# Kernel optimization log

Hardware: AMD Instinct MI355X
Metric: run time of the kernel (lower is better)

Reference implementation:

```python
import jax, jax.numpy as jnp
import numpy as np

N = 4096        # atoms
F = 128         # node feature channels (MACE hidden irreps scalar channels)
K = 8           # radial basis size
NELEM = 10      # chemical elements
RMAX = 5.0      # cutoff (Angstrom), model.r_max
BOX = 34.5      # box side -> ~0.1 atoms/A^3, ~50 neighbors within RMAX


def setup_inputs() -> dict:
    key = jax.random.key(0)
    ks = jax.random.split(key, 7)
    positions = jax.random.uniform(ks[0], (N, 3), jnp.float32) * BOX
    z = jax.random.randint(ks[1], (N,), 0, NELEM)
    embed = jax.random.normal(ks[2], (NELEM, F), jnp.float32) * 0.1
    W1 = jax.random.normal(ks[3], (K, F, F), jnp.float32) / np.sqrt(K * F)
    W2 = jax.random.normal(ks[4], (K, F, F), jnp.float32) / np.sqrt(K * F)
    Wr1 = jax.random.normal(ks[5], (F, F), jnp.float32) / np.sqrt(F)
    Wr2 = jax.random.normal(ks[6], (F, 1), jnp.float32) / np.sqrt(F)
    return dict(positions=positions, z=z, embed=embed, W1=W1, W2=W2, Wr1=Wr1, Wr2=Wr2)


def _energy(positions, embed, W1, W2, Wr1, Wr2, z):
    # node embedding from atomic species (node_attrs one-hot @ embedding)
    h = embed[z]                                            # [N,F]
    # --- neighborlist: radius graph with self-edge masking (pbc = False) ---
    sq = jnp.sum(positions * positions, axis=-1)            # [N]
    d2 = sq[:, None] + sq[None, :] - 2.0 * (positions @ positions.T)  # [N,N]
    eye = jnp.eye(positions.shape[0], dtype=bool)
    d2_safe = jnp.where(eye | (d2 <= 0), 1.0, d2)           # avoid sqrt(0) grad
    d = jnp.sqrt(d2_safe)                                   # [N,N]
    mask = (d < RMAX) & (~eye) & (d2 > 0)                   # keep_edge = ~true_self_edge
    # smooth cutoff envelope
    env = jnp.where(mask, 0.5 * (jnp.cos(jnp.pi * d / RMAX) + 1.0), 0.0)  # [N,N]
    # Gaussian radial basis
    mus = jnp.linspace(0.0, RMAX, K, dtype=jnp.float32)     # [K]
    gamma = jnp.float32((K / RMAX) ** 2)
    rbf = jnp.exp(-gamma * (d[..., None] - mus) ** 2) * env[..., None]    # [N,N,K]
    # --- two message-passing layers (radial-weighted neighbor aggregation) ---
    for W in (W1, W2):
        A = jnp.einsum('ijk,jf->ikf', rbf, h)               # [N,K,F] gather-scatter agg
        h = jax.nn.silu(jnp.einsum('ikf,kfg->ig', A, W) + h)  # [N,F]
    # --- per-atom energy readout, summed over graph ---
    e_atom = (jax.nn.silu(h @ Wr1) @ Wr2)[:, 0]             # [N]
    return jnp.sum(e_atom)


def reference(positions, z, embed, W1, W2, Wr1, Wr2):
    energy, dE_dpos = jax.value_and_grad(_energy)(positions, embed, W1, W2, Wr1, Wr2, z)
    forces = -dE_dpos                                       # [N,3]
    return energy, forces
```

## Files before the change

kernel.cpp:

```cpp
#include <hip/hip_runtime.h>
#include <math.h>

#define N_ATOMS 4096
#define F 128
#define K 8
#define KF 1024
#define KFF 131072
#define FF 16384
#define NF 524288
#define NKF 4194304
#define MAXNB 128
#define RMAX 5.0f
#define GAMMA 2.56f
#define MU_STEP 0.714285714285714f
#define PI_F 3.14159265358979323846f
#define POR (PI_F / RMAX)

typedef __bf16 bf16x8_t __attribute__((ext_vector_type(8)));
typedef float f32x4_t __attribute__((ext_vector_type(4)));
typedef unsigned short u16x8_t __attribute__((ext_vector_type(8)));
typedef unsigned short u16x4_t __attribute__((ext_vector_type(4)));

__device__ __forceinline__ float sigm(float x){ return 1.0f/(1.0f + expf(-x)); }
__device__ __forceinline__ unsigned short f2bf(float x){
  unsigned int u = __float_as_uint(x);
  u += 0x7fff + ((u >> 16) & 1);
  return (unsigned short)(u >> 16);
}


__device__ __forceinline__ void agg_body(int a, int t,
        const float* __restrict__ h_in, const int* __restrict__ nb_idx,
        const float* __restrict__ rbf, const int* __restrict__ nb_cnt,
        unsigned short* __restrict__ Af){
  int grp = t >> 6, lane = t & 63;
  __shared__ int s_j[MAXNB];
  __shared__ float s_acc[4][8][128];
  int cnt = nb_cnt[a];
  for (int idx = t; idx < cnt; idx += 256) s_j[idx] = nb_idx[a*MAXNB + idx];
  __syncthreads();
  float2 acc[8];
  #pragma unroll
  for (int k = 0; k < 8; k++) acc[k] = {0.f, 0.f};
  const float4* rb = (const float4*)(rbf + (size_t)a*MAXNB*8);
  for (int n = grp; n < cnt; n += 4){
    float2 hv = *(const float2*)&h_in[(size_t)s_j[n]*F + lane*2];
    float4 r0 = rb[n*2], r1 = rb[n*2+1];
    acc[0].x += r0.x*hv.x; acc[0].y += r0.x*hv.y;
    acc[1].x += r0.y*hv.x; acc[1].y += r0.y*hv.y;
    acc[2].x += r0.z*hv.x; acc[2].y += r0.z*hv.y;
    acc[3].x += r0.w*hv.x; acc[3].y += r0.w*hv.y;
    acc[4].x += r1.x*hv.x; acc[4].y += r1.x*hv.y;
    acc[5].x += r1.y*hv.x; acc[5].y += r1.y*hv.y;
    acc[6].x += r1.z*hv.x; acc[6].y += r1.z*hv.y;
    acc[7].x += r1.w*hv.x; acc[7].y += r1.w*hv.y;
  }
  #pragma unroll
  for (int k = 0; k < 8; k++)
    *(float2*)&s_acc[grp][k][lane*2] = acc[k];
  __syncthreads();
  int k = t >> 5, q = t & 31;
  int f0 = q*4;
  float v[4];
  #pragma unroll
  for (int i = 0; i < 4; i++){
    int f = f0 + i;
    v[i] = s_acc[0][k][f] + s_acc[1][k][f] + s_acc[2][k][f] + s_acc[3][k][f];
  }
  int lf = (a & 15) | (((f0 >> 3) & 3) << 4);
  int kc = k*4 + (f0 >> 5);
  size_t flat = (size_t)(a >> 4)*16384 + ((size_t)kc*64 + lf)*8 + (f0 & 7);
  u16x4_t o;
  o[0] = f2bf(v[0]); o[1] = f2bf(v[1]); o[2] = f2bf(v[2]); o[3] = f2bf(v[3]);
  *(u16x4_t*)(Af + flat) = o;
}

__device__ __forceinline__ void mgemm_bwd_body(int bx, int t,
        const unsigned short* __restrict__ Gf, const unsigned short* __restrict__ Bf,
        unsigned short* __restrict__ dAbf){
  int l = t & 63, w = t >> 6;
  int rtile = (bx & 63)*4 + w;
  int nt0 = (bx >> 6)*8;
  f32x4_t acc[8];
  #pragma unroll
  for (int i = 0; i < 8; i++) acc[i] = (f32x4_t){0.f,0.f,0.f,0.f};
  const unsigned short* Ab = Gf + (size_t)rtile*2048 + l*8;
  const unsigned short* Bb = Bf + l*8;
  #pragma unroll
  for (int kc = 0; kc < 4; kc++){
    bf16x8_t a = *(const bf16x8_t*)(Ab + kc*512);
    #pragma unroll
    for (int nt = 0; nt < 8; nt++){
      bf16x8_t b = *(const bf16x8_t*)(Bb + (kc*64 + nt0 + nt)*512);
      acc[nt] = __builtin_amdgcn_mfma_f32_16x16x32_bf16(a, b, acc[nt], 0, 0, 0);
    }
  }
  int row0 = rtile*16 + (l >> 4)*4;
  int col = l & 15;
  #pragma unroll
  for (int nt = 0; nt < 8; nt++){
    #pragma unroll
    for (int r = 0; r < 4; r++)
      dAbf[(size_t)(row0+r)*1024 + (nt0+nt)*16 + col] = f2bf(acc[nt][r]);
  }
}


__global__ __launch_bounds__(256) void k_prep(const float* __restrict__ pos,
        const int* __restrict__ z, const float* __restrict__ embed,
        const float* __restrict__ W1, const float* __restrict__ W2,
        const float* __restrict__ Wr1,
        int* __restrict__ nb_idx, float* __restrict__ nb_d, int* __restrict__ nb_cnt,
        float* __restrict__ rbf, float* __restrict__ drbf,
        unsigned short* __restrict__ WF1, unsigned short* __restrict__ WF2,
        unsigned short* __restrict__ WDF2, unsigned short* __restrict__ WTF1,
        unsigned short* __restrict__ WTF2, unsigned short* __restrict__ Wr1F,
        unsigned short* __restrict__ Wr1TF,
        float* __restrict__ h0, unsigned short* __restrict__ h0bf){
  int t = threadIdx.x;
  if (blockIdx.x < 1024){
    int w = t >> 6, lane = t & 63;
    int i = blockIdx.x*4 + w;
    __shared__ float spx[256], spy[256], spz[256], ssq[256];
    float pix = pos[3*i], piy = pos[3*i+1], piz = pos[3*i+2];
    float sqi = pix*pix + piy*piy + piz*piz;
    int count = 0;
    for (int jb = 0; jb < N_ATOMS; jb += 256){
      __syncthreads();
      float px = pos[3*(jb+t)], py = pos[3*(jb+t)+1], pz = pos[3*(jb+t)+2];
      spx[t] = px; spy[t] = py; spz[t] = pz;
      ssq[t] = px*px + py*py + pz*pz;
      __syncthreads();
      #pragma unroll
      for (int c = 0; c < 4; c++){
        int jj = c*64 + lane;
        int j = jb + jj;
        float dot = pix*spx[jj] + piy*spy[jj] + piz*spz[jj];
        float d2 = sqi + ssq[jj] - 2.0f*dot;
        float d = sqrtf(d2);
        bool pred = (j != i) && (d2 > 0.0f) && (d < RMAX);
        unsigned long long m = __ballot(pred);
        int off = __popcll(m & ((1ull << lane) - 1ull));
        if (pred){
          int p = count + off;
          if (p < MAXNB){ nb_idx[i*MAXNB + p] = j; nb_d[i*MAXNB + p] = d; }
        }
        count += __popcll(m);
      }
    }
    int cc = count > MAXNB ? MAXNB : count;
    if (lane == 0) nb_cnt[i] = cc;
    __syncthreads();
    for (int n = lane; n < cc; n += 64){
      float d = nb_d[i*MAXNB + n];
      float ph = POR*d;
      float cph, sph;
      __sincosf(ph, &sph, &cph);
      float env = 0.5f*(cph + 1.0f);
      float denv = -0.5f*POR*sph;
      float rr[8], dd[8];
      #pragma unroll
      for (int k = 0; k < 8; k++){
        float dm = d - MU_STEP*(float)k;
        float G = expf(-GAMMA*dm*dm);
        rr[k] = G*env;
        dd[k] = G*(-2.0f*GAMMA*dm*env + denv);
      }
      float4* rb = (float4*)(rbf + ((size_t)i*MAXNB + n)*8);
      rb[0] = {rr[0],rr[1],rr[2],rr[3]};
      rb[1] = {rr[4],rr[5],rr[6],rr[7]};
      float4* db = (float4*)(drbf + ((size_t)i*MAXNB + n)*8);
      db[0] = {dd[0],dd[1],dd[2],dd[3]};
      db[1] = {dd[4],dd[5],dd[6],dd[7]};
    }
    return;
  }
  if (blockIdx.x >= 1088){
    int idx = (blockIdx.x - 1088)*256 + t;
    int i = idx >> 7, f = idx & 127;
    float v = embed[z[i]*F + f];
    h0[idx] = v;
    h0bf[idx] = f2bf(v);
    return;
  }
  int idx = (blockIdx.x - 1024)*256 + t;
  int l = idx & 63;
  int hi = idx >> 6;
  {
    int kc = hi >> 3, nt = hi & 7;
    int kfb = kc*32 + ((l>>4)&3)*8;
    int g = nt*16 + (l&15);
    u16x8_t v1, v2, vd;
    #pragma unroll
    for (int j = 0; j < 8; j++){
      int kf = kfb + j;
      v1[j] = f2bf(W1[kf*128 + g]);
      v2[j] = f2bf(W2[kf*128 + g]);
      vd[j] = f2bf(W2[(kf>>7)*FF + g*F + (kf&127)]);
    }
    *(u16x8_t*)(WF1 + idx*8) = v1;
    *(u16x8_t*)(WF2 + idx*8) = v2;
    *(u16x8_t*)(WDF2 + idx*8) = vd;
  }
  {
    int kc = hi >> 6, nt = hi & 63;
    int gb = kc*32 + ((l>>4)&3)*8;
    int kf = nt*16 + (l&15);
    u16x8_t t1, t2;
    #pragma unroll
    for (int j = 0; j < 8; j++){
      int g = gb + j;
      t1[j] = f2bf(W1[kf*128 + g]);
      t2[j] = f2bf(W2[kf*128 + g]);
    }
    *(u16x8_t*)(WTF1 + idx*8) = t1;
    *(u16x8_t*)(WTF2 + idx*8) = t2;
  }
  {
    int m = idx >> 9;
    int ll = (idx >> 3) & 63;
    int j = idx & 7;
    int kc = m >> 3, nt = m & 7;
    int kf = kc*32 + ((ll>>4)&3)*8 + j;
    int g = nt*16 + (ll&15);
    Wr1F[idx]  = f2bf(Wr1[kf*128 + g]);
    Wr1TF[idx] = f2bf(Wr1[g*128 + kf]);
  }
}

__global__ __launch_bounds__(256) void k_agg(const float* __restrict__ h_in,
        const int* __restrict__ nb_idx, const float* __restrict__ rbf,
        const int* __restrict__ nb_cnt, unsigned short* __restrict__ Af){
  agg_body(blockIdx.x, threadIdx.x, h_in, nb_idx, rbf, nb_cnt, Af);
}

__global__ __launch_bounds__(256) void k_bwdmix(const unsigned short* __restrict__ Gf,
        const unsigned short* __restrict__ Bf, unsigned short* __restrict__ dAbf,
        const float* __restrict__ g2b, const int* __restrict__ nb_idx,
        const float* __restrict__ rbf, const int* __restrict__ nb_cnt,
        unsigned short* __restrict__ Af){
  if (blockIdx.x < 512){
    mgemm_bwd_body(blockIdx.x, threadIdx.x, Gf, Bf, dAbf);
    return;
  }
  agg_body(blockIdx.x - 512, threadIdx.x, g2b, nb_idx, rbf, nb_cnt, Af);
}

__global__ __launch_bounds__(256) void k_mgemm_bwd(const unsigned short* __restrict__ Gf,
        const unsigned short* __restrict__ Bf, unsigned short* __restrict__ dAbf){
  mgemm_bwd_body(blockIdx.x, threadIdx.x, Gf, Bf, dAbf);
}

__global__ __launch_bounds__(256) void k_mgemm_fwd(const unsigned short* __restrict__ Af,
        const unsigned short* __restrict__ Bf, const float* __restrict__ addv,
        const float* __restrict__ msrc, float* __restrict__ out_m,
        float* __restrict__ out_h, unsigned short* __restrict__ out_hbf,
        unsigned short* __restrict__ out_frag, int mode){
  int t = threadIdx.x;
  int l = t & 63, w = t >> 6;
  int rtile = blockIdx.x;
  int nt = blockIdx.y*4 + w;
  f32x4_t accA = (f32x4_t){0.f,0.f,0.f,0.f};
  f32x4_t accB = (f32x4_t){0.f,0.f,0.f,0.f};
  const unsigned short* Ab = Af + (size_t)rtile*16384 + l*8;
  const unsigned short* Bb = Bf + l*8;
  #pragma unroll
  for (int kc = 0; kc < 32; kc += 2){
    bf16x8_t a0 = *(const bf16x8_t*)(Ab + kc*512);
    bf16x8_t b0 = *(const bf16x8_t*)(Bb + (kc*8 + nt)*512);
    bf16x8_t a1 = *(const bf16x8_t*)(Ab + (kc+1)*512);
    bf16x8_t b1 = *(const bf16x8_t*)(Bb + ((kc+1)*8 + nt)*512);
    accA = __builtin_amdgcn_mfma_f32_16x16x32_bf16(a0, b0, accA, 0, 0, 0);
    accB = __builtin_amdgcn_mfma_f32_16x16x32_bf16(a1, b1, accB, 0, 0, 0);
  }
  f32x4_t acc = accA + accB;
  int row0 = rtile*16 + (l >> 4)*4;
  int col = nt*16 + (l & 15);
  if (mode == 0){
    #pragma unroll
    for (int r = 0; r < 4; r++){
      int i = row0 + r;
      float m = acc[r] + addv[(size_t)i*F + col];
      out_m[(size_t)i*F + col] = m;
      float h = m*sigm(m);
      out_h[(size_t)i*F + col] = h;
      out_hbf[(size_t)i*F + col] = f2bf(h);
    }
  } else {
    int kc2 = col >> 5;
    int lfr0 = (((col >> 3) & 3) << 4);
    int jj = col & 7;
    #pragma unroll
    for (int r = 0; r < 4; r++){
      int i = row0 + r;
      float mm = msrc[(size_t)i*F + col];
      float sg = sigm(mm);
      float gv = (acc[r] + addv[(size_t)i*F + col])*(sg*(1.f + mm*(1.f - sg)));
      int lfr = (i & 15) | lfr0;
      size_t flat = (((size_t)(i>>4)*4 + kc2)*64 + lfr)*8 + jj;
      out_frag[flat] = f2bf(gv);
    }
  }
}

__global__ __launch_bounds__(64) void k_readout(const unsigned short* __restrict__ h2bf,
        const float* __restrict__ m2, const unsigned short* __restrict__ Wr1F,
        const unsigned short* __restrict__ Wr1TF, const float* __restrict__ Wr2,
        float* __restrict__ e_at, float* __restrict__ g2,
        unsigned short* __restrict__ g2frag){
  int a0 = blockIdx.x*16;
  int l = threadIdx.x;
  int rl = l & 15;
  __shared__ unsigned short sdu[16][136];
  f32x4_t acc[8];
  #pragma unroll
  for (int nt = 0; nt < 8; nt++) acc[nt] = (f32x4_t){0.f,0.f,0.f,0.f};
  #pragma unroll
  for (int kc = 0; kc < 4; kc++){
    bf16x8_t af = *(const bf16x8_t*)(h2bf + (size_t)(a0+rl)*F + kc*32 + ((l>>4)&3)*8);
    #pragma unroll
    for (int nt = 0; nt < 8; nt++){
      bf16x8_t bf = *(const bf16x8_t*)(Wr1F + ((kc*8+nt)*64 + l)*8);
      acc[nt] = __builtin_amdgcn_mfma_f32_16x16x32_bf16(af, bf, acc[nt], 0, 0, 0);
    }
  }
  float epart[4] = {0.f,0.f,0.f,0.f};
  #pragma unroll
  for (int nt = 0; nt < 8; nt++){
    float w2 = Wr2[nt*16 + rl];
    #pragma unroll
    for (int r = 0; r < 4; r++){
      float u = acc[nt][r];
      float sg = sigm(u);
      epart[r] += u*sg*w2;
      sdu[(l>>4)*4 + r][nt*16 + rl] = f2bf(w2*(sg*(1.f + u*(1.f - sg))));
    }
  }
  #pragma unroll
  for (int o = 1; o < 16; o <<= 1){
    #pragma unroll
    for (int r = 0; r < 4; r++) epart[r] += __shfl_xor(epart[r], o);
  }
  if (rl == 0){
    #pragma unroll
    for (int r = 0; r < 4; r++) e_at[a0 + (l>>4)*4 + r] = epart[r];
  }
  __syncthreads();
  f32x4_t acc2[8];
  #pragma unroll
  for (int nt = 0; nt < 8; nt++) acc2[nt] = (f32x4_t){0.f,0.f,0.f,0.f};
  #pragma unroll
  for (int kc = 0; kc < 4; kc++){
    bf16x8_t af = *(const bf16x8_t*)&sdu[rl][kc*32 + ((l>>4)&3)*8];
    #pragma unroll
    for (int nt = 0; nt < 8; nt++){
      bf16x8_t bf = *(const bf16x8_t*)(Wr1TF + ((kc*8+nt)*64 + l)*8);
      acc2[nt] = __builtin_amdgcn_mfma_f32_16x16x32_bf16(af, bf, acc2[nt], 0, 0, 0);
    }
  }
  #pragma unroll
  for (int nt = 0; nt < 8; nt++){
    int g = nt*16 + rl;
    int kc2 = g >> 5;
    int lfr0 = (((g >> 3) & 3) << 4);
    int jj = g & 7;
    #pragma unroll
    for (int r = 0; r < 4; r++){
      int a = a0 + (l>>4)*4 + r;
      float mm = m2[(size_t)a*F + g];
      float sg = sigm(mm);
      float gv = acc2[nt][r]*(sg*(1.f + mm*(1.f - sg)));
      g2[(size_t)a*F + g] = gv;
      int lfr = (a & 15) | lfr0;
      g2frag[(((size_t)(a>>4)*4 + kc2)*64 + lfr)*8 + jj] = f2bf(gv);
    }
  }
}

__global__ __launch_bounds__(256) void k_edge(const unsigned short* __restrict__ dA2bf,
        const unsigned short* __restrict__ dA1bf, const unsigned short* __restrict__ h1bf,
        const unsigned short* __restrict__ h0bf, const float* __restrict__ drbf,
        const int* __restrict__ nb_idx, const int* __restrict__ nb_cnt,
        float* __restrict__ edge_s){
  int a = blockIdx.x;
  int t = threadIdx.x;
  int w = t >> 6, l = t & 63;
  __shared__ int s_j[MAXNB];
  int cnt = nb_cnt[a];
  for (int idx = t; idx < cnt; idx += 256) s_j[idx] = nb_idx[a*MAXNB + idx];
  int r = l & 15;
  int sel = (l >> 4) & 3;
  u16x8_t a2u[4], a1u[4];
  #pragma unroll
  for (int kc = 0; kc < 4; kc++){
    u16x8_t v2 = {0,0,0,0,0,0,0,0};
    u16x8_t v1 = {0,0,0,0,0,0,0,0};
    if (r < 8){
      v2 = *(const u16x8_t*)(dA2bf + (size_t)a*KF + r*F + kc*32 + sel*8);
      v1 = *(const u16x8_t*)(dA1bf + (size_t)a*KF + r*F + kc*32 + sel*8);
    }
    a2u[kc] = v2; a1u[kc] = v1;
  }
  __syncthreads();
  for (int n0 = w*16; n0 < cnt; n0 += 64){
    int nl = n0 + r;
    int nls = nl < cnt ? nl : cnt - 1;
    int j = s_j[nls];
    const unsigned short* h1p = h1bf + (size_t)j*F + sel*8;
    const unsigned short* h0p = h0bf + (size_t)j*F + sel*8;
    f32x4_t acc = (f32x4_t){0.f,0.f,0.f,0.f};
    #pragma unroll
    for (int kc = 0; kc < 4; kc++){
      bf16x8_t b = *(const bf16x8_t*)(h1p + kc*32);
      acc = __builtin_amdgcn_mfma_f32_16x16x32_bf16(*(const bf16x8_t*)&a2u[kc], b, acc, 0, 0, 0);
    }
    #pragma unroll
    for (int kc = 0; kc < 4; kc++){
      bf16x8_t b = *(const bf16x8_t*)(h0p + kc*32);
      acc = __builtin_amdgcn_mfma_f32_16x16x32_bf16(*(const bf16x8_t*)&a1u[kc], b, acc, 0, 0, 0);
    }
    int krow = (l >> 4) * 4;
    float part = 0.f;
    if (krow < 8){
      float4 dr = *(const float4*)(drbf + ((size_t)a*MAXNB + nls)*8 + krow);
      part = acc[0]*dr.x + acc[1]*dr.y + acc[2]*dr.z + acc[3]*dr.w;
    }
    part += __shfl_xor(part, 16);
    if (l < 16 && nl < cnt) edge_s[a*MAXNB + nl] = part;
  }
}

__global__ __launch_bounds__(64) void k_force(const float* __restrict__ pos,
        const int* __restrict__ nb_idx, const float* __restrict__ nb_d,
        const int* __restrict__ nb_cnt, const float* __restrict__ edge_s,
        const float* __restrict__ e_at, float* __restrict__ out){
  int a = blockIdx.x;
  int lane = threadIdx.x;
  if (a == N_ATOMS){
    float s = 0.f;
    for (int i = lane; i < N_ATOMS; i += 64) s += e_at[i];
    #pragma unroll
    for (int o = 1; o < 64; o <<= 1) s += __shfl_xor(s, o);
    if (lane == 0) out[0] = s;
    return;
  }
  float pax = pos[3*a], pay = pos[3*a+1], paz = pos[3*a+2];
  int cnt = nb_cnt[a];
  float fx = 0.f, fy = 0.f, fz = 0.f;
  for (int n = lane; n < cnt; n += 64){
    int j = nb_idx[a*MAXNB + n];
    float d = nb_d[a*MAXNB + n];
    float s = edge_s[a*MAXNB + n];
    int cj = nb_cnt[j];
    int lo = 0, hi = cj - 1, p = -1;
    while (lo <= hi){
      int mid = (lo + hi) >> 1;
      int v = nb_idx[j*MAXNB + mid];
      if (v == a){ p = mid; break; }
      if (v < a) lo = mid + 1; else hi = mid - 1;
    }
    float sj = (p >= 0) ? edge_s[j*MAXNB + p] : 0.0f;
    float coef = (s + sj)/d;
    float dx = pax - pos[3*j], dy = pay - pos[3*j+1], dz = paz - pos[3*j+2];
    fx -= coef*dx; fy -= coef*dy; fz -= coef*dz;
  }
  #pragma unroll
  for (int o = 1; o < 64; o <<= 1){
    fx += __shfl_xor(fx, o); fy += __shfl_xor(fy, o); fz += __shfl_xor(fz, o);
  }
  if (lane == 0){
    out[1 + 3*a + 0] = fx;
    out[1 + 3*a + 1] = fy;
    out[1 + 3*a + 2] = fz;
  }
}

extern "C" void kernel_launch(void* const* d_in, const int* in_sizes, int n_in,
                              void* d_out, int out_size, void* d_ws, size_t ws_size,
                              hipStream_t stream){
  const float* pos   = (const float*)d_in[0];
  const int*   z     = (const int*)  d_in[1];
  const float* embed = (const float*)d_in[2];
  const float* W1    = (const float*)d_in[3];
  const float* W2    = (const float*)d_in[4];
  const float* Wr1   = (const float*)d_in[5];
  const float* Wr2   = (const float*)d_in[6];
  float* out = (float*)d_out;

  float* ws = (float*)d_ws;
  float* h0   = ws;
  float* h1   = h0 + NF;
  float* h2   = h1 + NF;
  float* m1   = h2 + NF;
  float* m2   = m1 + NF;
  float* g2b  = m2 + NF;
  float* Bbuf = g2b + NF;
  float* Cbuf = Bbuf + NKF;
  unsigned short* dA2bf = (unsigned short*)Bbuf;
  unsigned short* dA1bf = (unsigned short*)Cbuf;
  unsigned short* Afrag = (unsigned short*)(Cbuf + NKF);
  unsigned short* Gfrag = Afrag + NKF;
  unsigned short* h0bf = Gfrag + NF;
  unsigned short* h1bf = h0bf + NF;
  unsigned short* h2bf = h1bf + NF;
  unsigned short* WF1  = h2bf + NF;
  unsigned short* WF2  = WF1 + KFF;
  unsigned short* WDF2 = WF2 + KFF;
  unsigned short* WTF1 = WDF2 + KFF;
  unsigned short* WTF2 = WTF1 + KFF;
  unsigned short* Wr1F  = WTF2 + KFF;
  unsigned short* Wr1TF = Wr1F + FF;
  float* e_at = (float*)(Wr1TF + FF);
  float* nb_d = e_at + N_ATOMS;
  float* edge_s = nb_d + N_ATOMS*MAXNB;
  float* rbf  = edge_s + N_ATOMS*MAXNB;
  float* drbf = rbf + N_ATOMS*MAXNB*8;
  int* nb_idx = (int*)(drbf + N_ATOMS*MAXNB*8);
  int* nb_cnt = nb_idx + N_ATOMS*MAXNB;

  k_prep<<<1024 + 64 + NF/256, 256, 0, stream>>>(pos, z, embed, W1, W2, Wr1,
        nb_idx, nb_d, nb_cnt, rbf, drbf,
        WF1, WF2, WDF2, WTF1, WTF2, Wr1F, Wr1TF, h0, h0bf);

  k_agg<<<N_ATOMS, 256, 0, stream>>>(h0, nb_idx, rbf, nb_cnt, Afrag);
  k_mgemm_fwd<<<dim3(256, 2), 256, 0, stream>>>(Afrag, WF1, h0, h0, m1, h1, h1bf, Gfrag, 0);
  k_agg<<<N_ATOMS, 256, 0, stream>>>(h1, nb_idx, rbf, nb_cnt, Afrag);
  k_mgemm_fwd<<<dim3(256, 2), 256, 0, stream>>>(Afrag, WF2, h1, h1, m2, h2, h2bf, Gfrag, 0);

  k_readout<<<N_ATOMS/16, 64, 0, stream>>>(h2bf, m2, Wr1F, Wr1TF, Wr2, e_at, g2b, Gfrag);

  k_bwdmix<<<512 + N_ATOMS, 256, 0, stream>>>(Gfrag, WTF2, dA2bf,
        g2b, nb_idx, rbf, nb_cnt, Afrag);
  k_mgemm_fwd<<<dim3(256, 2), 256, 0, stream>>>(Afrag, WDF2, g2b, m1, m1, m1, h2bf, Gfrag, 1);
  k_mgemm_bwd<<<512, 256, 0, stream>>>(Gfrag, WTF1, dA1bf);
  k_edge<<<N_ATOMS, 256, 0, stream>>>(dA2bf, dA1bf, h1bf, h0bf, drbf, nb_idx, nb_cnt, edge_s);
  k_force<<<N_ATOMS + 1, 64, 0, stream>>>(pos, nb_idx, nb_d, nb_cnt, edge_s, e_at, out);
}
```

Before: 187.9 us.

## Replace all-pairs neighbor search with cell-list binning and sorted per-atom scan

Swaps the O(N^2) brute-force radius search for a 6x6x6 cell grid. Atoms are binned with atomics in the prep kernel, then a new per-atom kernel scans only the 27 neighboring cells. It bitonic-sorts each neighbor list by index to keep the original deterministic ordering, then computes rbf/drbf. This adds a memset and an extra launch, and any cell with more than 64 atoms would silently drop neighbors.

```diff
diff --git a/kernel.cpp b/kernel.cpp
--- a/kernel.cpp
+++ b/kernel.cpp
@@ -15,6 +15,10 @@
 #define MU_STEP 0.714285714285714f
 #define PI_F 3.14159265358979323846f
 #define POR (PI_F / RMAX)
+#define NCELL 6
+#define NCELL3 216
+#define CELLCAP 64
+#define CINV 0.1739130434782609f
 
 typedef __bf16 bf16x8_t __attribute__((ext_vector_type(8)));
 typedef float f32x4_t __attribute__((ext_vector_type(4)));
@@ -110,80 +114,33 @@
         const int* __restrict__ z, const float* __restrict__ embed,
         const float* __restrict__ W1, const float* __restrict__ W2,
         const float* __restrict__ Wr1,
-        int* __restrict__ nb_idx, float* __restrict__ nb_d, int* __restrict__ nb_cnt,
-        float* __restrict__ rbf, float* __restrict__ drbf,
+        int* __restrict__ cell_cnt, int* __restrict__ cell_list,
         unsigned short* __restrict__ WF1, unsigned short* __restrict__ WF2,
         unsigned short* __restrict__ WDF2, unsigned short* __restrict__ WTF1,
         unsigned short* __restrict__ WTF2, unsigned short* __restrict__ Wr1F,
         unsigned short* __restrict__ Wr1TF,
         float* __restrict__ h0, unsigned short* __restrict__ h0bf){
   int t = threadIdx.x;
-  if (blockIdx.x < 1024){
-    int w = t >> 6, lane = t & 63;
-    int i = blockIdx.x*4 + w;
-    __shared__ float spx[256], spy[256], spz[256], ssq[256];
-    float pix = pos[3*i], piy = pos[3*i+1], piz = pos[3*i+2];
-    float sqi = pix*pix + piy*piy + piz*piz;
-    int count = 0;
-    for (int jb = 0; jb < N_ATOMS; jb += 256){
-      __syncthreads();
-      float px = pos[3*(jb+t)], py = pos[3*(jb+t)+1], pz = pos[3*(jb+t)+2];
-      spx[t] = px; spy[t] = py; spz[t] = pz;
-      ssq[t] = px*px + py*py + pz*pz;
-      __syncthreads();
-      #pragma unroll
-      for (int c = 0; c < 4; c++){
-        int jj = c*64 + lane;
-        int j = jb + jj;
-        float dot = pix*spx[jj] + piy*spy[jj] + piz*spz[jj];
-        float d2 = sqi + ssq[jj] - 2.0f*dot;
-        float d = sqrtf(d2);
-        bool pred = (j != i) && (d2 > 0.0f) && (d < RMAX);
-        unsigned long long m = __ballot(pred);
-        int off = __popcll(m & ((1ull << lane) - 1ull));
-        if (pred){
-          int p = count + off;
-          if (p < MAXNB){ nb_idx[i*MAXNB + p] = j; nb_d[i*MAXNB + p] = d; }
-        }
-        count += __popcll(m);
-      }
-    }
-    int cc = count > MAXNB ? MAXNB : count;
-    if (lane == 0) nb_cnt[i] = cc;
-    __syncthreads();
-    for (int n = lane; n < cc; n += 64){
-      float d = nb_d[i*MAXNB + n];
-      float ph = POR*d;
-      float cph, sph;
-      __sincosf(ph, &sph, &cph);
-      float env = 0.5f*(cph + 1.0f);
-      float denv = -0.5f*POR*sph;
-      float rr[8], dd[8];
-      #pragma unroll
-      for (int k = 0; k < 8; k++){
-        float dm = d - MU_STEP*(float)k;
-        float G = expf(-GAMMA*dm*dm);
-        rr[k] = G*env;
-        dd[k] = G*(-2.0f*GAMMA*dm*env + denv);
-      }
-      float4* rb = (float4*)(rbf + ((size_t)i*MAXNB + n)*8);
-      rb[0] = {rr[0],rr[1],rr[2],rr[3]};
-      rb[1] = {rr[4],rr[5],rr[6],rr[7]};
-      float4* db = (float4*)(drbf + ((size_t)i*MAXNB + n)*8);
-      db[0] = {dd[0],dd[1],dd[2],dd[3]};
-      db[1] = {dd[4],dd[5],dd[6],dd[7]};
-    }
+  if (blockIdx.x < 16){
+    int i = blockIdx.x*256 + t;
+    float x = pos[3*i], y = pos[3*i+1], zz = pos[3*i+2];
+    int cx = (int)(x*CINV); cx = cx > 5 ? 5 : (cx < 0 ? 0 : cx);
+    int cy = (int)(y*CINV); cy = cy > 5 ? 5 : (cy < 0 ? 0 : cy);
+    int cz = (int)(zz*CINV); cz = cz > 5 ? 5 : (cz < 0 ? 0 : cz);
+    int c = (cz*NCELL + cy)*NCELL + cx;
+    int slot = atomicAdd(&cell_cnt[c], 1);
+    if (slot < CELLCAP) cell_list[c*CELLCAP + slot] = i;
     return;
   }
-  if (blockIdx.x >= 1088){
-    int idx = (blockIdx.x - 1088)*256 + t;
+  if (blockIdx.x >= 80){
+    int idx = (blockIdx.x - 80)*256 + t;
     int i = idx >> 7, f = idx & 127;
     float v = embed[z[i]*F + f];
     h0[idx] = v;
     h0bf[idx] = f2bf(v);
     return;
   }
-  int idx = (blockIdx.x - 1024)*256 + t;
+  int idx = (blockIdx.x - 16)*256 + t;
   int l = idx & 63;
   int hi = idx >> 6;
   {
@@ -225,6 +182,96 @@
     int g = nt*16 + (ll&15);
     Wr1F[idx]  = f2bf(Wr1[kf*128 + g]);
     Wr1TF[idx] = f2bf(Wr1[g*128 + kf]);
+  }
+}
+
+__global__ __launch_bounds__(64) void k_nbscan(const float* __restrict__ pos,
+        const int* __restrict__ cell_cnt, const int* __restrict__ cell_list,
+        int* __restrict__ nb_idx, float* __restrict__ nb_d, int* __restrict__ nb_cnt,
+        float* __restrict__ rbf, float* __restrict__ drbf){
+  int a = blockIdx.x;
+  int lane = threadIdx.x;
+  __shared__ int s_jb[128];
+  __shared__ float s_db[128];
+  float pax = pos[3*a], pay = pos[3*a+1], paz = pos[3*a+2];
+  int cx = (int)(pax*CINV); cx = cx > 5 ? 5 : (cx < 0 ? 0 : cx);
+  int cy = (int)(pay*CINV); cy = cy > 5 ? 5 : (cy < 0 ? 0 : cy);
+  int cz = (int)(paz*CINV); cz = cz > 5 ? 5 : (cz < 0 ? 0 : cz);
+  int cnt = 0;
+  for (int dz = -1; dz <= 1; dz++){
+    int zc = cz + dz; if (zc < 0 || zc >= NCELL) continue;
+    for (int dy = -1; dy <= 1; dy++){
+      int yc = cy + dy; if (yc < 0 || yc >= NCELL) continue;
+      for (int dx = -1; dx <= 1; dx++){
+        int xc = cx + dx; if (xc < 0 || xc >= NCELL) continue;
+        int c = (zc*NCELL + yc)*NCELL + xc;
+        int m = cell_cnt[c];
+        if (m > CELLCAP) m = CELLCAP;
+        for (int base = 0; base < m; base += 64){
+          int idx = base + lane;
+          int j = -1; float d = 0.f; bool pred = false;
+          if (idx < m){
+            j = cell_list[c*CELLCAP + idx];
+            float dxp = pax - pos[3*j], dyp = pay - pos[3*j+1], dzp = paz - pos[3*j+2];
+            float d2 = dxp*dxp + dyp*dyp + dzp*dzp;
+            d = sqrtf(d2);
+            pred = (j != a) && (d2 > 0.0f) && (d < RMAX);
+          }
+          unsigned long long mm = __ballot(pred);
+          int off = __popcll(mm & ((1ull << lane) - 1ull));
+          if (pred && (cnt + off) < 128){ s_jb[cnt+off] = j; s_db[cnt+off] = d; }
+          cnt += __popcll(mm);
+        }
+      }
+    }
+  }
+  if (cnt > MAXNB) cnt = MAXNB;
+  for (int s = cnt + lane; s < 128; s += 64){ s_jb[s] = 0x7fffffff; s_db[s] = 1e9f; }
+  __syncthreads();
+  for (int k = 2; k <= 128; k <<= 1){
+    for (int jj = k >> 1; jj > 0; jj >>= 1){
+      #pragma unroll
+      for (int sbase = 0; sbase < 128; sbase += 64){
+        int s = sbase + lane;
+        int partner = s ^ jj;
+        if (partner > s){
+          bool up = (s & k) == 0;
+          int j1 = s_jb[s], j2 = s_jb[partner];
+          bool sw = up ? (j1 > j2) : (j1 < j2);
+          if (sw){
+            float d1 = s_db[s], d2v = s_db[partner];
+            s_jb[s] = j2; s_jb[partner] = j1;
+            s_db[s] = d2v; s_db[partner] = d1;
+          }
+        }
+      }
+      __syncthreads();
+    }
+  }
+  if (lane == 0) nb_cnt[a] = cnt;
+  for (int n = lane; n < cnt; n += 64){
+    nb_idx[a*MAXNB + n] = s_jb[n];
+    nb_d[a*MAXNB + n]  = s_db[n];
+    float d = s_db[n];
+    float ph = POR*d;
+    float cph, sph;
+    __sincosf(ph, &sph, &cph);
+    float env = 0.5f*(cph + 1.0f);
+    float denv = -0.5f*POR*sph;
+    float rr[8], dd[8];
+    #pragma unroll
+    for (int k = 0; k < 8; k++){
+      float dm = d - MU_STEP*(float)k;
+      float G = expf(-GAMMA*dm*dm);
+      rr[k] = G*env;
+      dd[k] = G*(-2.0f*GAMMA*dm*env + denv);
+    }
+    float4* rb = (float4*)(rbf + ((size_t)a*MAXNB + n)*8);
+    rb[0] = {rr[0],rr[1],rr[2],rr[3]};
+    rb[1] = {rr[4],rr[5],rr[6],rr[7]};
+    float4* db = (float4*)(drbf + ((size_t)a*MAXNB + n)*8);
+    db[0] = {dd[0],dd[1],dd[2],dd[3]};
+    db[1] = {dd[4],dd[5],dd[6],dd[7]};
   }
 }
 
@@ -517,10 +564,15 @@
   float* drbf = rbf + N_ATOMS*MAXNB*8;
   int* nb_idx = (int*)(drbf + N_ATOMS*MAXNB*8);
   int* nb_cnt = nb_idx + N_ATOMS*MAXNB;
-
-  k_prep<<<1024 + 64 + NF/256, 256, 0, stream>>>(pos, z, embed, W1, W2, Wr1,
-        nb_idx, nb_d, nb_cnt, rbf, drbf,
+  int* cell_cnt = nb_cnt + N_ATOMS;
+  int* cell_list = cell_cnt + NCELL3;
+
+  hipMemsetAsync(cell_cnt, 0, NCELL3*sizeof(int), stream);
+  k_prep<<<16 + 64 + NF/256, 256, 0, stream>>>(pos, z, embed, W1, W2, Wr1,
+        cell_cnt, cell_list,
         WF1, WF2, WDF2, WTF1, WTF2, Wr1F, Wr1TF, h0, h0bf);
+  k_nbscan<<<N_ATOMS, 64, 0, stream>>>(pos, cell_cnt, cell_list,
+        nb_idx, nb_d, nb_cnt, rbf, drbf);
 
   k_agg<<<N_ATOMS, 256, 0, stream>>>(h0, nb_idx, rbf, nb_cnt, Afrag);
   k_mgemm_fwd<<<dim3(256, 2), 256, 0, stream>>>(Afrag, WF1, h0, h0, m1, h1, h1bf, Gfrag, 0);
```

Result: slower. 196.7 us (+4.7%).
